# Performance work log

Measured on AMD Instinct MI355X. Metric: run time of the kernel, lower is better.

## Reference

```python
import jax, jax.numpy as jnp
import numpy as np

B, T, C, H = 2, 2048, 1024, 16
DH = C // H
EPS = 1e-5

def _ln(x, g, b):
    mu = jnp.mean(x, axis=-1, keepdims=True)
    var = jnp.var(x, axis=-1, keepdims=True)
    return (x - mu) * jax.lax.rsqrt(var + EPS) * g + b

def setup_inputs() -> dict:
    key = jax.random.key(0)
    ks = jax.random.split(key, 6)
    s = 0.02
    return {
        "x": jax.random.normal(ks[0], (B, T, C), jnp.float32),
        "W_attn": jax.random.normal(ks[1], (C, 3 * C), jnp.float32) * s,
        "b_attn": jnp.zeros((3 * C,), jnp.float32),
        "W_o": jax.random.normal(ks[2], (C, C), jnp.float32) * s,
        "b_o": jnp.zeros((C,), jnp.float32),
        "W_fc": jax.random.normal(ks[3], (C, 4 * C), jnp.float32) * s,
        "b_fc": jnp.zeros((4 * C,), jnp.float32),
        "W_fc2": jax.random.normal(ks[4], (4 * C, C), jnp.float32) * s,
        "b_fc2": jnp.zeros((C,), jnp.float32),
        "g1": jnp.ones((C,), jnp.float32),
        "beta1": jnp.zeros((C,), jnp.float32),
        "g2": jnp.ones((C,), jnp.float32),
        "beta2": jnp.zeros((C,), jnp.float32),
    }

def reference(x, W_attn, b_attn, W_o, b_o, W_fc, b_fc, W_fc2, b_fc2, g1, beta1, g2, beta2):
    # --- causal self-attention on pre-normed input ---
    h = _ln(x, g1, beta1)
    qkv = h @ W_attn + b_attn                       # [B,T,3C]
    q, k, v = jnp.split(qkv, 3, axis=-1)
    q = q.reshape(B, T, H, DH).transpose(0, 2, 1, 3)  # [B,H,T,DH]
    k = k.reshape(B, T, H, DH).transpose(0, 2, 1, 3)
    v = v.reshape(B, T, H, DH).transpose(0, 2, 1, 3)
    att = jnp.einsum('bhqd,bhkd->bhqk', q, k) * (1.0 / np.sqrt(DH))
    mask = jnp.tril(jnp.ones((T, T), bool))
    att = jnp.where(mask, att, -jnp.inf)
    att = jax.nn.softmax(att, axis=-1)               # [B,H,T,T]
    y = jnp.einsum('bhqk,bhkd->bhqd', att, v)
    y = y.transpose(0, 2, 1, 3).reshape(B, T, C)
    scores = y @ W_o + b_o
    x = x + scores
    # --- MLP ---
    h2 = _ln(x, g2, beta2)
    m = jax.nn.gelu(h2 @ W_fc + b_fc, approximate=False)
    x = x + (m @ W_fc2 + b_fc2)
    return (x, att)
```

## Files before the change

### kernel.cpp

```cpp
#include <hip/hip_runtime.h>
#include <math.h>

#define BB  2
#define TT  2048
#define CC  1024
#define HH  16
#define DHD 64
#define MM  (BB*TT)

typedef unsigned short u16;
typedef __bf16 bf16t;
typedef bf16t bf16x8 __attribute__((ext_vector_type(8)));
typedef float f32x4 __attribute__((ext_vector_type(4)));

__device__ __forceinline__ u16 f2bf(float f) {
    union { float f; unsigned int u; } v; v.f = f;
    unsigned int r = v.u + 0x7fffu + ((v.u >> 16) & 1u);
    return (u16)(r >> 16);
}

__device__ __forceinline__ float bf2f(unsigned int u) {
    union { unsigned int u; float f; } v; v.u = u << 16;
    return v.f;
}

__device__ __forceinline__ f32x4 mfma16(bf16x8 a, bf16x8 b, f32x4 c) {
    return __builtin_amdgcn_mfma_f32_16x16x32_bf16(a, b, c, 0, 0, 0);
}

__device__ __forceinline__ void gload_lds16(const u16* g, u16* l) {
    __builtin_amdgcn_global_load_lds(
        (const __attribute__((address_space(1))) void*)g,
        (__attribute__((address_space(3))) void*)l, 16, 0, 0);
}

__global__ __launch_bounds__(256)
void prep_kernel(const float* __restrict__ W_attn, const float* __restrict__ W_o,
                 const float* __restrict__ W_fc,   const float* __restrict__ W_fc2,
                 u16* __restrict__ Wt_attn, u16* __restrict__ Wt_o,
                 u16* __restrict__ Wt_fc,   u16* __restrict__ Wt_fc2,
                 const float* __restrict__ x, const float* __restrict__ g1,
                 const float* __restrict__ bta, u16* __restrict__ h_out) {
    __shared__ float tile[32][33];
    __shared__ float ps[4], ps2[4];
    __shared__ float mu_s, rs_s;
    const int tid = threadIdx.x;
    int b = blockIdx.x;

    if (b < 12288) {
        const float* src; u16* dst; int R, Cc, bx, by;
        if (b < 3072)      {            src = W_attn; dst = Wt_attn; R = 1024; Cc = 3072; bx = b % 96;  by = b / 96; }
        else if (b < 4096) { b -= 3072; src = W_o;    dst = Wt_o;    R = 1024; Cc = 1024; bx = b % 32;  by = b / 32; }
        else if (b < 8192) { b -= 4096; src = W_fc;   dst = Wt_fc;   R = 1024; Cc = 4096; bx = b % 128; by = b / 128; }
        else               { b -= 8192; src = W_fc2;  dst = Wt_fc2;  R = 4096; Cc = 1024; bx = b % 32;  by = b / 32; }
        int tx = tid & 31, ty = tid >> 5;
        int c0 = bx * 32, r0 = by * 32;
        #pragma unroll
        for (int k = 0; k < 4; k++)
            tile[ty + 8*k][tx] = src[(size_t)(r0 + ty + 8*k) * Cc + c0 + tx];
        __syncthreads();
        #pragma unroll
        for (int k = 0; k < 4; k++)
            dst[(size_t)(c0 + ty + 8*k) * R + r0 + tx] = f2bf(tile[tx][ty + 8*k]);
        return;
    }

    const int row = b - 12288;
    const float* xr = x + (size_t)row * CC;
    float4 v = *(const float4*)(xr + tid * 4);
    float s  = v.x + v.y + v.z + v.w;
    float s2 = v.x*v.x + v.y*v.y + v.z*v.z + v.w*v.w;
    for (int o = 32; o > 0; o >>= 1) {
        s  += __shfl_down(s,  o, 64);
        s2 += __shfl_down(s2, o, 64);
    }
    int wv = tid >> 6, lane = tid & 63;
    if (lane == 0) { ps[wv] = s; ps2[wv] = s2; }
    __syncthreads();
    if (tid == 0) {
        float st  = ps[0] + ps[1] + ps[2] + ps[3];
        float st2 = ps2[0] + ps2[1] + ps2[2] + ps2[3];
        float mu = st / (float)CC;
        float var = st2 / (float)CC - mu * mu;
        mu_s = mu; rs_s = rsqrtf(var + 1e-5f);
    }
    __syncthreads();
    float mu = mu_s, rs = rs_s;
    float4 gv = *(const float4*)(g1 + tid * 4);
    float4 bv = *(const float4*)(bta + tid * 4);
    u16 o0 = f2bf((v.x - mu) * rs * gv.x + bv.x);
    u16 o1 = f2bf((v.y - mu) * rs * gv.y + bv.y);
    u16 o2 = f2bf((v.z - mu) * rs * gv.z + bv.z);
    u16 o3 = f2bf((v.w - mu) * rs * gv.w + bv.w);
    uint2 pk;
    pk.x = (unsigned)o0 | ((unsigned)o1 << 16);
    pk.y = (unsigned)o2 | ((unsigned)o3 << 16);
    *(uint2*)(h_out + (size_t)row * CC + tid * 4) = pk;
}

__global__ __launch_bounds__(256)
void ln_kernel(const float* __restrict__ x, const float* __restrict__ g,
               const float* __restrict__ bta, u16* __restrict__ out) {
    const int row = blockIdx.x;
    const int tid = threadIdx.x;
    const float* xr = x + (size_t)row * CC;
    float4 v = *(const float4*)(xr + tid * 4);
    float s  = v.x + v.y + v.z + v.w;
    float s2 = v.x*v.x + v.y*v.y + v.z*v.z + v.w*v.w;
    for (int o = 32; o > 0; o >>= 1) {
        s  += __shfl_down(s,  o, 64);
        s2 += __shfl_down(s2, o, 64);
    }
    __shared__ float ps[4], ps2[4];
    __shared__ float mu_s, rs_s;
    int wv = tid >> 6, lane = tid & 63;
    if (lane == 0) { ps[wv] = s; ps2[wv] = s2; }
    __syncthreads();
    if (tid == 0) {
        float st  = ps[0] + ps[1] + ps[2] + ps[3];
        float st2 = ps2[0] + ps2[1] + ps2[2] + ps2[3];
        float mu = st / (float)CC;
        float var = st2 / (float)CC - mu * mu;
        mu_s = mu; rs_s = rsqrtf(var + 1e-5f);
    }
    __syncthreads();
    float mu = mu_s, rs = rs_s;
    float4 gv = *(const float4*)(g + tid * 4);
    float4 bv = *(const float4*)(bta + tid * 4);
    u16 o0 = f2bf((v.x - mu) * rs * gv.x + bv.x);
    u16 o1 = f2bf((v.y - mu) * rs * gv.y + bv.y);
    u16 o2 = f2bf((v.z - mu) * rs * gv.z + bv.z);
    u16 o3 = f2bf((v.w - mu) * rs * gv.w + bv.w);
    uint2 pk;
    pk.x = (unsigned)o0 | ((unsigned)o1 << 16);
    pk.y = (unsigned)o2 | ((unsigned)o3 << 16);
    *(uint2*)(out + (size_t)row * CC + tid * 4) = pk;
}

template<int EPI, bool NARROW>
__global__ __launch_bounds__(256, 2)
void gemm_kernel(const u16* __restrict__ A, int lda,
                 const u16* __restrict__ Bt, int ldb,
                 const float* __restrict__ bias,
                 const float* __restrict__ resid,
                 void* __restrict__ out, int N, int K,
                 u16* __restrict__ vtout) {
    constexpr int BN = NARROW ? 64 : 128;
    constexpr int NI = NARROW ? 2 : 4;
    __shared__ __align__(16) u16 As[128 * 64];
    __shared__ __align__(16) u16 Bs[BN * 64];
    const int tid = threadIdx.x;
    const int wv = tid >> 6, lane = tid & 63;
    const int ln = lane & 15, q4 = lane >> 4;
    const int l7 = ln & 7;
    const int sw0 = (q4 ^ l7) * 8;
    const int sw1 = ((4 + q4) ^ l7) * 8;
    const int m_blk = blockIdx.y * 128, n_blk = blockIdx.x * BN;
    const int wr = NARROW ? (wv * 32) : ((wv >> 1) * 64);
    const int wc = NARROW ? 0 : ((wv & 1) * 64);

    f32x4 acc[NI][4];
    #pragma unroll
    for (int i = 0; i < NI; i++)
        #pragma unroll
        for (int j = 0; j < 4; j++) acc[i][j] = (f32x4){0.f, 0.f, 0.f, 0.f};

    for (int kb = 0; kb < K; kb += 64) {
        __syncthreads();
        #pragma unroll
        for (int it = 0; it < 4; it++) {
            int b = it * 256 + tid;
            int row = b >> 3, c = b & 7;
            int cg = c ^ (row & 7);
            gload_lds16(A + (size_t)(m_blk + row) * lda + kb + cg * 8, As + b * 8);
        }
        #pragma unroll
        for (int it = 0; it < BN / 32; it++) {
            int b = it * 256 + tid;
            int row = b >> 3, c = b & 7;
            int cg = c ^ (row & 7);
            gload_lds16(Bt + (size_t)(n_blk + row) * ldb + kb + cg * 8, Bs + b * 8);
        }
        __syncthreads();
        #pragma unroll
        for (int kk = 0; kk < 2; kk++) {
            const int sw = kk ? sw1 : sw0;
            bf16x8 af[NI], bfr[4];
            #pragma unroll
            for (int i = 0; i < NI; i++)
                af[i] = *(const bf16x8*)(As + (wr + 16*i + ln) * 64 + sw);
            #pragma unroll
            for (int j = 0; j < 4; j++)
                bfr[j] = *(const bf16x8*)(Bs + (wc + 16*j + ln) * 64 + sw);
            #pragma unroll
            for (int i = 0; i < NI; i++)
                #pragma unroll
                for (int j = 0; j < 4; j++)
                    acc[i][j] = mfma16(af[i], bfr[j], acc[i][j]);
        }
    }

    #pragma unroll
    for (int i = 0; i < NI; i++) {
        #pragma unroll
        for (int j = 0; j < 4; j++) {
            int colb = n_blk + wc + 16*j + ln;
            if (EPI == 3 && colb >= 2048) {
                int hd = (colb - 2048) >> 6, dh = (colb - 2048) & 63;
                int row0 = m_blk + wr + 16*i + 4*q4;
                int bb = row0 >> 11, t = row0 & 2047;
                float bcol = bias[colb];
                uint2 pk;
                pk.x = (unsigned)f2bf(acc[i][j][0] + bcol)
                     | ((unsigned)f2bf(acc[i][j][1] + bcol) << 16);
                pk.y = (unsigned)f2bf(acc[i][j][2] + bcol)
                     | ((unsigned)f2bf(acc[i][j][3] + bcol) << 16);
                *(uint2*)(vtout + (((size_t)(bb * 16 + hd)) * 64 + dh) * TT + t) = pk;
                continue;
            }
            #pragma unroll
            for (int r = 0; r < 4; r++) {
                int row = m_blk + wr + 16*i + 4*q4 + r;
                int col = colb;
                float v = acc[i][j][r] + bias[col];
                if (EPI == 0 || EPI == 3) {
                    ((u16*)out)[(size_t)row * N + col] = f2bf(v);
                } else if (EPI == 1) {
                    ((float*)out)[(size_t)row * N + col] = v + resid[(size_t)row * N + col];
                } else if (EPI == 2) {
                    float gl = 0.5f * v * (1.0f + erff(v * 0.70710678118654752f));
                    ((u16*)out)[(size_t)row * N + col] = f2bf(gl);
                }
            }
        }
    }
}

__global__ __launch_bounds__(256, 2)
void attn_kernel(const u16* __restrict__ qkv, const u16* __restrict__ vt,
                 float* __restrict__ att_out, u16* __restrict__ y_ws) {
    __shared__ __align__(16) u16 Qs[128 * 64];
    __shared__ __align__(16) u16 Ks[2][64 * 64];
    __shared__ __align__(16) u16 Vs[2][64 * 64];
    __shared__ __align__(16) u16 Ps[128 * 72];
    const int tid = threadIdx.x;
    const int wv = tid >> 6, lane = tid & 63;
    const int ln = lane & 15, q4 = lane >> 4;
    const int l7 = ln & 7;
    const int sw0 = (q4 ^ l7) * 8;
    const int sw1 = ((4 + q4) ^ l7) * 8;
    const int bx = blockIdx.x;
    const int qt = (bx < 256) ? (15 - (bx >> 5)) : ((bx - 256) >> 5);
    const int bh = bx & 31, bb = bh >> 4, hd = bh & 15;

    const u16* Qg = qkv + ((size_t)(bb * TT) + qt * 128) * 3072 + hd * 64;
    const u16* Kg = qkv + (size_t)(bb * TT) * 3072 + 1024 + hd * 64;
    const u16* Vg = vt + (size_t)bh * 64 * TT;
    float* att = att_out + (size_t)bh * TT * TT + (size_t)(qt * 128) * TT;

    #pragma unroll
    for (int it = 0; it < 4; it++) {
        int b = it * 256 + tid;
        int row = b >> 3, c = b & 7, cg = c ^ (row & 7);
        gload_lds16(Qg + (size_t)row * 3072 + cg * 8, Qs + b * 8);
    }
    #pragma unroll
    for (int it = 0; it < 2; it++) {
        int b = it * 256 + tid;
        int row = b >> 3, c = b & 7, cg = c ^ (row & 7);
        gload_lds16(Kg + (size_t)row * 3072 + cg * 8, Ks[0] + b * 8);
    }
    {
        int zstart = (qt + 1) * 128;
        int zc = TT - zstart;
        if (zc > 0) {
            int cpr = zc >> 2;
            int tot = 128 * cpr;
            for (int v = tid; v < tot; v += 256) {
                int row = v / cpr;
                int c4 = v - row * cpr;
                __builtin_nontemporal_store((f32x4){0.f, 0.f, 0.f, 0.f},
                    (f32x4*)(att + (size_t)row * TT + zstart + c4 * 4));
            }
        }
    }

    const int nkt = 2 * qt + 2;
    const float scale = 0.125f;

    __syncthreads();

    bf16x8 qa[2][2];
    #pragma unroll
    for (int rt = 0; rt < 2; rt++) {
        int qrow = 32*wv + 16*rt + ln;
        qa[rt][0] = *(const bf16x8*)(Qs + qrow * 64 + sw0);
        qa[rt][1] = *(const bf16x8*)(Qs + qrow * 64 + sw1);
    }

    float psum[2][4];
    #pragma unroll
    for (int rt = 0; rt < 2; rt++)
        #pragma unroll
        for (int r = 0; r < 4; r++) psum[rt][r] = 0.f;

    for (int kt = 0; kt < nkt; kt++) {
        if (kt + 1 < nkt) {
            u16* dst = Ks[(kt + 1) & 1];
            #pragma unroll
            for (int it = 0; it < 2; it++) {
                int b = it * 256 + tid;
                int row = b >> 3, c = b & 7, cg = c ^ (row & 7);
                gload_lds16(Kg + (size_t)((kt + 1) * 64 + row) * 3072 + cg * 8, dst + b * 8);
            }
        }
        const u16* Kb = Ks[kt & 1];
        #pragma unroll
        for (int rt = 0; rt < 2; rt++) {
            #pragma unroll
            for (int ct = 0; ct < 4; ct++) {
                int krow = 16*ct + ln;
                f32x4 s = (f32x4){0.f,0.f,0.f,0.f};
                bf16x8 b0 = *(const bf16x8*)(Kb + krow * 64 + sw0);
                bf16x8 b1 = *(const bf16x8*)(Kb + krow * 64 + sw1);
                s = mfma16(qa[rt][0], b0, s);
                s = mfma16(qa[rt][1], b1, s);
                #pragma unroll
                for (int r = 0; r < 4; r++) {
                    int rowg = qt * 128 + 32*wv + 16*rt + 4*q4 + r;
                    int colg = kt * 64 + 16*ct + ln;
                    psum[rt][r] += (colg <= rowg) ? __expf(s[r] * scale) : 0.f;
                }
            }
        }
        __syncthreads();
    }

    float inv_l[2][4];
    #pragma unroll
    for (int rt = 0; rt < 2; rt++)
        #pragma unroll
        for (int r = 0; r < 4; r++) {
            float t = psum[rt][r];
            for (int o = 1; o < 16; o <<= 1) t += __shfl_xor(t, o, 64);
            inv_l[rt][r] = 1.0f / t;
        }

    f32x4 acc_y[2][4];
    #pragma unroll
    for (int rt = 0; rt < 2; rt++)
        #pragma unroll
        for (int j = 0; j < 4; j++) acc_y[rt][j] = (f32x4){0.f,0.f,0.f,0.f};

    #pragma unroll
    for (int it = 0; it < 2; it++) {
        int b = it * 256 + tid;
        int row = b >> 3, c = b & 7, cg = c ^ (row & 7);
        gload_lds16(Kg + (size_t)row * 3072 + cg * 8, Ks[0] + b * 8);
        gload_lds16(Vg + (size_t)row * TT + cg * 8,   Vs[0] + b * 8);
    }
    __syncthreads();
    for (int kt = 0; kt < nkt; kt++) {
        if (kt + 1 < nkt) {
            u16* dk = Ks[(kt + 1) & 1];
            u16* dv = Vs[(kt + 1) & 1];
            #pragma unroll
            for (int it = 0; it < 2; it++) {
                int b = it * 256 + tid;
                int row = b >> 3, c = b & 7, cg = c ^ (row & 7);
                gload_lds16(Kg + (size_t)((kt + 1) * 64 + row) * 3072 + cg * 8, dk + b * 8);
                gload_lds16(Vg + (size_t)row * TT + (kt + 1) * 64 + cg * 8,     dv + b * 8);
            }
        }
        const u16* Kb = Ks[kt & 1];
        #pragma unroll
        for (int rt = 0; rt < 2; rt++) {
            #pragma unroll
            for (int ct = 0; ct < 4; ct++) {
                int krow = 16*ct + ln;
                f32x4 s = (f32x4){0.f,0.f,0.f,0.f};
                bf16x8 b0 = *(const bf16x8*)(Kb + krow * 64 + sw0);
                bf16x8 b1 = *(const bf16x8*)(Kb + krow * 64 + sw1);
                s = mfma16(qa[rt][0], b0, s);
                s = mfma16(qa[rt][1], b1, s);
                #pragma unroll
                for (int r = 0; r < 4; r++) {
                    int rowl = 32*wv + 16*rt + 4*q4 + r;
                    int rowg = qt * 128 + rowl;
                    int colg = kt * 64 + 16*ct + ln;
                    float p = (colg <= rowg)
                            ? __expf(s[r] * scale) * inv_l[rt][r] : 0.f;
                    Ps[rowl * 72 + 16*ct + ln] = f2bf(p);
                }
            }
        }
        const u16* Vb = Vs[kt & 1];
        #pragma unroll
        for (int kk = 0; kk < 2; kk++) {
            const int sw = kk ? sw1 : sw0;
            bf16x8 pa[2], vb[4];
            #pragma unroll
            for (int rt = 0; rt < 2; rt++)
                pa[rt] = *(const bf16x8*)(Ps + (32*wv + 16*rt + ln) * 72 + kk*32 + q4*8);
            #pragma unroll
            for (int j = 0; j < 4; j++)
                vb[j] = *(const bf16x8*)(Vb + (16*j + ln) * 64 + sw);
            #pragma unroll
            for (int rt = 0; rt < 2; rt++)
                #pragma unroll
                for (int j = 0; j < 4; j++)
                    acc_y[rt][j] = mfma16(pa[rt], vb[j], acc_y[rt][j]);
        }
        {
            float* attb = att + kt * 64;
            #pragma unroll
            for (int rr = 0; rr < 8; rr++) {
                int rowl = 32*wv + 4*rr + q4;
                uint2 pk = *(const uint2*)(Ps + rowl * 72 + ln * 4);
                f32x4 w;
                w[0] = bf2f(pk.x & 0xffffu);
                w[1] = bf2f(pk.x >> 16);
                w[2] = bf2f(pk.y & 0xffffu);
                w[3] = bf2f(pk.y >> 16);
                __builtin_nontemporal_store(w,
                    (f32x4*)(attb + (size_t)rowl * TT + ln * 4));
            }
        }
        __syncthreads();
    }

    #pragma unroll
    for (int rt = 0; rt < 2; rt++)
        #pragma unroll
        for (int j = 0; j < 4; j++)
            #pragma unroll
            for (int r = 0; r < 4; r++) {
                int rowl = 32*wv + 16*rt + 4*q4 + r;
                int t = qt * 128 + rowl;
                int dh = 16*j + ln;
                y_ws[((size_t)(bb * TT + t)) * CC + hd * DHD + dh] = f2bf(acc_y[rt][j][r]);
            }
}

extern "C" void kernel_launch(void* const* d_in, const int* in_sizes, int n_in,
                              void* d_out, int out_size, void* d_ws, size_t ws_size,
                              hipStream_t stream) {
    const float* x      = (const float*)d_in[0];
    const float* W_attn = (const float*)d_in[1];
    const float* b_attn = (const float*)d_in[2];
    const float* W_o    = (const float*)d_in[3];
    const float* b_o    = (const float*)d_in[4];
    const float* W_fc   = (const float*)d_in[5];
    const float* b_fc   = (const float*)d_in[6];
    const float* W_fc2  = (const float*)d_in[7];
    const float* b_fc2  = (const float*)d_in[8];
    const float* g1     = (const float*)d_in[9];
    const float* beta1  = (const float*)d_in[10];
    const float* g2     = (const float*)d_in[11];
    const float* beta2  = (const float*)d_in[12];

    char* ws = (char*)d_ws;
    u16* Wt_attn = (u16*)(ws);
    u16* Wt_o    = (u16*)(ws + 6291456);
    u16* Wt_fc   = (u16*)(ws + 8388608);
    u16* Wt_fc2  = (u16*)(ws + 16777216);
    u16* h_ws    = (u16*)(ws + 25165824);
    u16* qkv_ws  = (u16*)(ws + 33554432);
    u16* vt_ws   = (u16*)(ws + 58720256);
    u16* y_ws    = (u16*)(ws + 67108864);
    u16* m_ws    = (u16*)(ws + 33554432);

    float* out_x = (float*)d_out;
    float* att   = (float*)d_out + (size_t)BB * TT * CC;

    prep_kernel<<<dim3(16384), 256, 0, stream>>>(
        W_attn, W_o, W_fc, W_fc2, Wt_attn, Wt_o, Wt_fc, Wt_fc2,
        x, g1, beta1, h_ws);

    gemm_kernel<3, false><<<dim3(3072/128, MM/128), 256, 0, stream>>>(
        h_ws, 1024, Wt_attn, 1024, b_attn, nullptr, qkv_ws, 3072, 1024, vt_ws);

    attn_kernel<<<dim3(512), 256, 0, stream>>>(qkv_ws, vt_ws, att, y_ws);

    gemm_kernel<1, true><<<dim3(1024/64, MM/128), 256, 0, stream>>>(
        y_ws, 1024, Wt_o, 1024, b_o, x, out_x, 1024, 1024, nullptr);

    ln_kernel<<<MM, 256, 0, stream>>>(out_x, g2, beta2, h_ws);

    gemm_kernel<2, false><<<dim3(4096/128, MM/128), 256, 0, stream>>>(
        h_ws, 1024, Wt_fc, 1024, b_fc, nullptr, m_ws, 4096, 1024, nullptr);

    gemm_kernel<1, true><<<dim3(1024/64, MM/128), 256, 0, stream>>>(
        m_ws, 4096, Wt_fc2, 4096, b_fc2, out_x, out_x, 1024, 4096, nullptr);
}
```

Baseline: 823.9 us.

## Double-buffer LDS tiles in GEMM kernel to overlap global loads with MFMA

The GEMM main loop now keeps two LDS buffers for the A and B tiles. It preloads the first K-tile before the loop, then issues the global-to-LDS loads for the next tile before computing on the current one, with one barrier per iteration instead of two. The aim is to hide global load latency behind the MFMA work. In exchange, LDS use per block doubles, which could limit occupancy. If the compiler inserts a conservative wait on outstanding loads before the LDS reads, the overlap may not happen.

```diff
diff --git a/kernel.cpp b/kernel.cpp
--- a/kernel.cpp
+++ b/kernel.cpp
@@ -147,8 +147,8 @@
                  u16* __restrict__ vtout) {
     constexpr int BN = NARROW ? 64 : 128;
     constexpr int NI = NARROW ? 2 : 4;
-    __shared__ __align__(16) u16 As[128 * 64];
-    __shared__ __align__(16) u16 Bs[BN * 64];
+    __shared__ __align__(16) u16 As[2][128 * 64];
+    __shared__ __align__(16) u16 Bs[2][BN * 64];
     const int tid = threadIdx.x;
     const int wv = tid >> 6, lane = tid & 63;
     const int ln = lane & 15, q4 = lane >> 4;
@@ -159,45 +159,67 @@
     const int wr = NARROW ? (wv * 32) : ((wv >> 1) * 64);
     const int wc = NARROW ? 0 : ((wv & 1) * 64);
 
+    const int sb  = tid;
+    const int arow = sb >> 3, ac = sb & 7;
+    const int acg = ac ^ (arow & 7);
+
     f32x4 acc[NI][4];
     #pragma unroll
     for (int i = 0; i < NI; i++)
         #pragma unroll
         for (int j = 0; j < 4; j++) acc[i][j] = (f32x4){0.f, 0.f, 0.f, 0.f};
 
+    #pragma unroll
+    for (int it = 0; it < 4; it++) {
+        int b = it * 256 + tid;
+        int row = b >> 3, c = b & 7, cg = c ^ (row & 7);
+        gload_lds16(A + (size_t)(m_blk + row) * lda + cg * 8, As[0] + b * 8);
+    }
+    #pragma unroll
+    for (int it = 0; it < BN / 32; it++) {
+        int b = it * 256 + tid;
+        int row = b >> 3, c = b & 7, cg = c ^ (row & 7);
+        gload_lds16(Bt + (size_t)(n_blk + row) * ldb + cg * 8, Bs[0] + b * 8);
+    }
+
+    int cur = 0;
     for (int kb = 0; kb < K; kb += 64) {
         __syncthreads();
-        #pragma unroll
-        for (int it = 0; it < 4; it++) {
-            int b = it * 256 + tid;
-            int row = b >> 3, c = b & 7;
-            int cg = c ^ (row & 7);
-            gload_lds16(A + (size_t)(m_blk + row) * lda + kb + cg * 8, As + b * 8);
-        }
-        #pragma unroll
-        for (int it = 0; it < BN / 32; it++) {
-            int b = it * 256 + tid;
-            int row = b >> 3, c = b & 7;
-            int cg = c ^ (row & 7);
-            gload_lds16(Bt + (size_t)(n_blk + row) * ldb + kb + cg * 8, Bs + b * 8);
-        }
-        __syncthreads();
+        if (kb + 64 < K) {
+            u16* ad = As[cur ^ 1];
+            u16* bd = Bs[cur ^ 1];
+            #pragma unroll
+            for (int it = 0; it < 4; it++) {
+                int b = it * 256 + tid;
+                int row = b >> 3, c = b & 7, cg = c ^ (row & 7);
+                gload_lds16(A + (size_t)(m_blk + row) * lda + kb + 64 + cg * 8, ad + b * 8);
+            }
+            #pragma unroll
+            for (int it = 0; it < BN / 32; it++) {
+                int b = it * 256 + tid;
+                int row = b >> 3, c = b & 7, cg = c ^ (row & 7);
+                gload_lds16(Bt + (size_t)(n_blk + row) * ldb + kb + 64 + cg * 8, bd + b * 8);
+            }
+        }
+        const u16* Ab = As[cur];
+        const u16* Bb = Bs[cur];
         #pragma unroll
         for (int kk = 0; kk < 2; kk++) {
             const int sw = kk ? sw1 : sw0;
             bf16x8 af[NI], bfr[4];
             #pragma unroll
             for (int i = 0; i < NI; i++)
-                af[i] = *(const bf16x8*)(As + (wr + 16*i + ln) * 64 + sw);
+                af[i] = *(const bf16x8*)(Ab + (wr + 16*i + ln) * 64 + sw);
             #pragma unroll
             for (int j = 0; j < 4; j++)
-                bfr[j] = *(const bf16x8*)(Bs + (wc + 16*j + ln) * 64 + sw);
+                bfr[j] = *(const bf16x8*)(Bb + (wc + 16*j + ln) * 64 + sw);
             #pragma unroll
             for (int i = 0; i < NI; i++)
                 #pragma unroll
                 for (int j = 0; j < 4; j++)
                     acc[i][j] = mfma16(af[i], bfr[j], acc[i][j]);
         }
+        cur ^= 1;
     }
 
     #pragma unroll
```

Measured after the change: 834.9 us. Within noise of the previous version (+1.3%).
